# Performance work log

Measured on AMD Instinct MI355X. Metric: run time of the kernel, lower is better.

Reference implementation:

```python
import jax, jax.numpy as jnp
import numpy as np
from jax import lax

GRID_SIZE = 5
SPLINE_ORDER = 3
N_COEF = GRID_SIZE + SPLINE_ORDER  # 8 b-spline basis functions per input
GRID_LO, GRID_HI = -1.0, 1.0


def _grid():
    h = (GRID_HI - GRID_LO) / GRID_SIZE
    return jnp.arange(-SPLINE_ORDER, GRID_SIZE + SPLINE_ORDER + 1, dtype=jnp.float32) * h + GRID_LO


def _bsplines(x):
    # x: [..., in] -> [..., in, N_COEF] via Cox-de Boor recursion (efficient-kan)
    grid = _grid()
    x = x[..., None]
    bases = ((x >= grid[:-1]) & (x < grid[1:])).astype(x.dtype)
    for j in range(1, SPLINE_ORDER + 1):
        bases = ((x - grid[:-(j + 1)]) / (grid[j:-1] - grid[:-(j + 1)]) * bases[..., :-1]
                 + (grid[j + 1:] - x) / (grid[j + 1:] - grid[1:-j]) * bases[..., 1:])
    return bases


def _kan_linear(x, base_w, spline_w):
    # x: [..., in]; base_w: [out, in]; spline_w: [out, in, N_COEF]
    base = jax.nn.silu(x) @ base_w.T
    b = _bsplines(x).reshape(x.shape[:-1] + (-1,))  # [..., in*N_COEF]
    return base + b @ spline_w.reshape(spline_w.shape[0], -1).T


def _kan_conv(x, base_w, spline_w):
    # x: [B, C, H, W]; 3x3 valid KAN convolution
    patches = lax.conv_general_dilated_patches(x, (3, 3), (1, 1), 'VALID')  # [B, C*9, H-2, W-2]
    p = patches.transpose(0, 2, 3, 1)  # [B, Ho, Wo, C*9]
    out = _kan_linear(p, base_w, spline_w)  # [B, Ho, Wo, out]
    return out.transpose(0, 3, 1, 2)


def _maxpool2(x):
    return lax.reduce_window(x, -jnp.inf, lax.max, (1, 1, 2, 2), (1, 1, 2, 2), 'VALID')


def setup_inputs() -> dict:
    key = jax.random.key(0)
    ks = jax.random.split(key, 12)
    B = 2048
    x = jax.random.uniform(ks[0], (B, 1, 28, 28), dtype=jnp.float32)
    s = 0.1
    return {
        'x': x,
        'bw1': jax.random.normal(ks[1], (5, 9), dtype=jnp.float32) * s,
        'sw1': jax.random.normal(ks[2], (5, 9, N_COEF), dtype=jnp.float32) * s,
        'bw2': jax.random.normal(ks[3], (5, 45), dtype=jnp.float32) * s,
        'sw2': jax.random.normal(ks[4], (5, 45, N_COEF), dtype=jnp.float32) * s,
        'bw3': jax.random.normal(ks[5], (2, 45), dtype=jnp.float32) * s,
        'sw3': jax.random.normal(ks[6], (2, 45, N_COEF), dtype=jnp.float32) * s,
        'w1': jax.random.normal(ks[7], (500, 162), dtype=jnp.float32) * 0.05,
        'b1': jnp.zeros((500,), dtype=jnp.float32),
        'w2': jax.random.normal(ks[8], (10, 500), dtype=jnp.float32) * 0.05,
        'b2': jnp.zeros((10,), dtype=jnp.float32),
    }


def reference(x, bw1, sw1, bw2, sw2, bw3, sw3, w1, b1, w2, b2):
    h = _kan_conv(x, bw1, sw1)       # [B, 5, 26, 26]
    h = _maxpool2(h)                 # [B, 5, 13, 13]
    h = _kan_conv(h, bw2, sw2)       # [B, 5, 11, 11]
    h = _kan_conv(h, bw3, sw3)       # [B, 2, 9, 9]
    h = h.reshape(h.shape[0], -1)    # [B, 162]
    h = jax.nn.relu(h @ w1.T + b1)   # [B, 500]
    return h @ w2.T + b2             # [B, 10]
```

## Files before the change

### kernel.cpp

```cpp
#include <hip/hip_runtime.h>


typedef _Float16 h2 __attribute__((ext_vector_type(2)));

__device__ __forceinline__ h2 u2h(unsigned int u) {
  union { unsigned int x; h2 h; } v; v.x = u; return v.h;
}
__device__ __forceinline__ unsigned short f2h_bits(float x) {
  union { _Float16 h; unsigned short u; } v; v.h = (_Float16)x; return v.u;
}
__device__ __forceinline__ unsigned int pack2h(float a, float b) {
  return (unsigned int)f2h_bits(a) | ((unsigned int)f2h_bits(b) << 16);
}
__device__ __forceinline__ float fdot2(h2 a, h2 b, float c) {
  return __builtin_amdgcn_fdot2(a, b, c, false);
}

__device__ __forceinline__ void featurize_regs(float v, uint4& bs, float& silu) {
  silu = v / (1.0f + __expf(-v));
  bs.x = 0u; bs.y = 0u; bs.z = 0u; bs.w = 0u;
  float u = fmaf(v, 2.5f, 5.5f);
  if (u >= 0.0f && u < 11.0f) {
    float tf = floorf(u);
    float f = u - tf, f2 = f * f, f3 = f2 * f, om = 1.0f - f;
    const float c6 = 1.0f / 6.0f;
    float w0 = om * om * om * c6;
    float w1 = (3.0f * f3 - 6.0f * f2 + 4.0f) * c6;
    float w2 = (-3.0f * f3 + 3.0f * f2 + 3.0f * f + 1.0f) * c6;
    float w3 = f3 * c6;
    unsigned long long w01 =
        (unsigned long long)f2h_bits(w0) |
        ((unsigned long long)f2h_bits(w1) << 16) |
        ((unsigned long long)f2h_bits(w2) << 32) |
        ((unsigned long long)f2h_bits(w3) << 48);
    int t = (int)tf;
    int s = 16 * t - 48;
    unsigned long long lo, hi;
    if (s >= 0) {
      lo = (s < 64) ? (w01 << s) : 0ull;
      hi = (s == 0) ? 0ull : ((s < 64) ? (w01 >> (64 - s)) : (w01 << (s - 64)));
    } else {
      lo = w01 >> (-s);
      hi = 0ull;
    }
    bs.x = (unsigned int)lo; bs.y = (unsigned int)(lo >> 32);
    bs.z = (unsigned int)hi; bs.w = (unsigned int)(hi >> 32);
  }
}

__global__ __launch_bounds__(256) void k_prep(
    const float* __restrict__ bw1, const float* __restrict__ sw1,
    const float* __restrict__ bw2, const float* __restrict__ sw2,
    const float* __restrict__ bw3, const float* __restrict__ sw3,
    const float* __restrict__ w1, const float* __restrict__ w2,
    unsigned int* __restrict__ V1s, float* __restrict__ V1b,
    unsigned int* __restrict__ V2s, float* __restrict__ V2b,
    unsigned int* __restrict__ V3s, float* __restrict__ V3b,
    unsigned int* __restrict__ W1p4, float* __restrict__ W2p) {
  int t = blockIdx.x * 256 + threadIdx.x;
  if (t < 180) {
    int p = t & 3, o = (t >> 2) % 5, in = t / 20;
    V1s[t] = pack2h(sw1[(o * 9 + in) * 8 + 2 * p], sw1[(o * 9 + in) * 8 + 2 * p + 1]);
  }
  if (t < 45)  { int o = t % 5, in = t / 5; V1b[t] = bw1[o * 9 + in]; }
  if (t < 900) {
    int p = t & 3, o = (t >> 2) % 5, in = t / 20;
    V2s[t] = pack2h(sw2[(o * 45 + in) * 8 + 2 * p], sw2[(o * 45 + in) * 8 + 2 * p + 1]);
  }
  if (t < 225) { int o = t % 5, in = t / 5; V2b[t] = bw2[o * 45 + in]; }
  if (t < 360) {
    int p = t & 3, o = (t >> 2) & 1, in = t / 8;
    V3s[t] = pack2h(sw3[(o * 45 + in) * 8 + 2 * p], sw3[(o * 45 + in) * 8 + 2 * p + 1]);
  }
  if (t < 90)  { int o = t % 2, in = t / 2; V3b[t] = bw3[o * 45 + in]; }
  if (t < 43008) {
    int j = t & 3, o = (t >> 2) & 511, kpq = t >> 11;
    int kp = kpq * 4 + j;
    W1p4[t] = (o < 500 && kp < 81)
                  ? pack2h(w1[o * 162 + 2 * kp], w1[o * 162 + 2 * kp + 1])
                  : 0u;
  }
  if (t < 5120) {
    int o = t >> 9, k = t & 511;
    W2p[t] = (k < 500) ? w2[o * 500 + k] : 0.0f;
  }
}

__global__ __launch_bounds__(64, 2) void k_fused(
    const float* __restrict__ x,
    const unsigned int* __restrict__ V1s, const float* __restrict__ V1b,
    const unsigned int* __restrict__ V2s, const float* __restrict__ V2b,
    const unsigned int* __restrict__ V3s, const float* __restrict__ V3b,
    const unsigned int* __restrict__ W1p4, const float* __restrict__ W2p,
    const float* __restrict__ b1, const float* __restrict__ b2,
    float* __restrict__ out) {
  __shared__ uint4 bas[845];
  __shared__ float slu[845];
  float*        basF = (float*)bas;
  unsigned int* hpk  = (unsigned int*)slu + 256;
  const int b = blockIdx.x;
  const int lane = threadIdx.x;

  for (int l = lane; l < 784; l += 64) {
    uint4 bs; float sl;
    featurize_regs(x[b * 784 + l], bs, sl);
    bas[l] = bs; slu[l] = sl;
  }

  float h1v[3][5];
  #pragma unroll 1
  for (int it = 0; it < 3; ++it) {
    int p = it * 64 + lane;
    if (p < 169) {
      int py = p / 13, px = p % 13;
      int r0 = py * 2, c0 = px * 2;
      float wacc[4][5];
      #pragma unroll
      for (int wi = 0; wi < 4; ++wi)
        #pragma unroll
        for (int o = 0; o < 5; ++o) wacc[wi][o] = 0.0f;
      #pragma unroll
      for (int r = 0; r < 4; ++r) {
        uint4 q[4]; float sl[4];
        #pragma unroll
        for (int c = 0; c < 4; ++c) {
          q[c]  = bas[(r0 + r) * 28 + c0 + c];
          sl[c] = slu[(r0 + r) * 28 + c0 + c];
        }
        #pragma unroll
        for (int c = 0; c < 4; ++c) {
          h2 a0 = u2h(q[c].x), a1 = u2h(q[c].y), a2 = u2h(q[c].z), a3 = u2h(q[c].w);
          #pragma unroll
          for (int dy = 0; dy < 2; ++dy) {
            #pragma unroll
            for (int dx = 0; dx < 2; ++dx) {
              int ky = r - dy, kx = c - dx;
              if (ky >= 0 && ky < 3 && kx >= 0 && kx < 3) {
                const unsigned int* wp = V1s + (ky * 3 + kx) * 20;
                const float* bp = V1b + (ky * 3 + kx) * 5;
                #pragma unroll
                for (int o = 0; o < 5; ++o) {
                  float acc = wacc[dy * 2 + dx][o];
                  acc = fdot2(a0, u2h(wp[o * 4 + 0]), acc);
                  acc = fdot2(a1, u2h(wp[o * 4 + 1]), acc);
                  acc = fdot2(a2, u2h(wp[o * 4 + 2]), acc);
                  acc = fdot2(a3, u2h(wp[o * 4 + 3]), acc);
                  wacc[dy * 2 + dx][o] = fmaf(sl[c], bp[o], acc);
                }
              }
            }
          }
        }
      }
      #pragma unroll
      for (int o = 0; o < 5; ++o)
        h1v[it][o] = fmaxf(fmaxf(wacc[0][o], wacc[1][o]),
                           fmaxf(wacc[2][o], wacc[3][o]));
    }
  }
  #pragma unroll 1
  for (int it = 0; it < 3; ++it) {
    int p = it * 64 + lane;
    if (p < 169) {
      #pragma unroll
      for (int o = 0; o < 5; ++o) {
        uint4 bs; float sl;
        featurize_regs(h1v[it][o], bs, sl);
        bas[o * 169 + p] = bs; slu[o * 169 + p] = sl;
      }
    }
  }

  float h2v[2][5];
  #pragma unroll 1
  for (int it = 0; it < 2; ++it) {
    int pos = it * 64 + lane;
    if (pos < 121) {
      int y = pos / 11, xx = pos % 11;
      float acc2[5];
      #pragma unroll
      for (int o = 0; o < 5; ++o) acc2[o] = 0.0f;
      #pragma unroll 1
      for (int cky = 0; cky < 15; ++cky) {
        int c = cky / 3, ky = cky % 3;
        int base = c * 169 + (y + ky) * 13 + xx;
        uint4 q0 = bas[base], q1 = bas[base + 1], q2 = bas[base + 2];
        float s0 = slu[base], s1 = slu[base + 1], s2 = slu[base + 2];
        uint4 wq[15]; float wb[15];
        const uint4* wp4 = (const uint4*)(V2s + cky * 60);
        const float* bp  = V2b + cky * 15;
        #pragma unroll
        for (int i = 0; i < 15; ++i) { wq[i] = wp4[i]; wb[i] = bp[i]; }
        #pragma unroll
        for (int kx = 0; kx < 3; ++kx) {
          uint4 q = (kx == 0) ? q0 : ((kx == 1) ? q1 : q2);
          float sl = (kx == 0) ? s0 : ((kx == 1) ? s1 : s2);
          h2 a0 = u2h(q.x), a1 = u2h(q.y), a2 = u2h(q.z), a3 = u2h(q.w);
          #pragma unroll
          for (int o = 0; o < 5; ++o) {
            uint4 w = wq[kx * 5 + o];
            float a = acc2[o];
            a = fdot2(a0, u2h(w.x), a);
            a = fdot2(a1, u2h(w.y), a);
            a = fdot2(a2, u2h(w.z), a);
            a = fdot2(a3, u2h(w.w), a);
            acc2[o] = fmaf(sl, wb[kx * 5 + o], a);
          }
        }
      }
      #pragma unroll
      for (int o = 0; o < 5; ++o) h2v[it][o] = acc2[o];
    }
  }
  #pragma unroll 1
  for (int it = 0; it < 2; ++it) {
    int pos = it * 64 + lane;
    if (pos < 121) {
      #pragma unroll
      for (int o = 0; o < 5; ++o) {
        uint4 bs; float sl;
        featurize_regs(h2v[it][o], bs, sl);
        bas[o * 121 + pos] = bs; slu[o * 121 + pos] = sl;
      }
    }
  }

  float h3v[2][2];
  #pragma unroll 1
  for (int it = 0; it < 2; ++it) {
    int pos = it * 64 + lane;
    if (pos < 81) {
      int y = pos / 9, xx = pos % 9;
      float acc3[2] = {0.f, 0.f};
      #pragma unroll 1
      for (int cky = 0; cky < 15; ++cky) {
        int c = cky / 3, ky = cky % 3;
        int base = c * 121 + (y + ky) * 11 + xx;
        uint4 q0 = bas[base], q1 = bas[base + 1], q2 = bas[base + 2];
        float s0 = slu[base], s1 = slu[base + 1], s2 = slu[base + 2];
        uint4 wq[6]; float wb[6];
        const uint4* wp4 = (const uint4*)(V3s + cky * 24);
        const float* bp  = V3b + cky * 6;
        #pragma unroll
        for (int i = 0; i < 6; ++i) { wq[i] = wp4[i]; wb[i] = bp[i]; }
        #pragma unroll
        for (int kx = 0; kx < 3; ++kx) {
          uint4 q = (kx == 0) ? q0 : ((kx == 1) ? q1 : q2);
          float sl = (kx == 0) ? s0 : ((kx == 1) ? s1 : s2);
          h2 a0 = u2h(q.x), a1 = u2h(q.y), a2 = u2h(q.z), a3 = u2h(q.w);
          #pragma unroll
          for (int o = 0; o < 2; ++o) {
            uint4 w = wq[kx * 2 + o];
            float a = acc3[o];
            a = fdot2(a0, u2h(w.x), a);
            a = fdot2(a1, u2h(w.y), a);
            a = fdot2(a2, u2h(w.z), a);
            a = fdot2(a3, u2h(w.w), a);
            acc3[o] = fmaf(sl, wb[kx * 2 + o], a);
          }
        }
      }
      h3v[it][0] = acc3[0]; h3v[it][1] = acc3[1];
    }
  }
  #pragma unroll 1
  for (int it = 0; it < 2; ++it) {
    int pos = it * 64 + lane;
    if (pos < 81) { slu[pos] = h3v[it][0]; slu[81 + pos] = h3v[it][1]; }
  }
  hpk[lane] = pack2h(slu[2 * lane], slu[2 * lane + 1]);
  {
    int i1 = 64 + lane;
    if (i1 < 84)
      hpk[i1] = (i1 < 81) ? pack2h(slu[2 * i1], slu[2 * i1 + 1]) : 0u;
  }

  float fa[8];
  #pragma unroll
  for (int i = 0; i < 8; ++i) fa[i] = 0.0f;
  {
    const uint4* hp4 = (const uint4*)hpk;
    #pragma unroll 1
    for (int kpq = 0; kpq < 21; ++kpq) {
      uint4 hk = hp4[kpq];
      const uint4* wrow = (const uint4*)W1p4 + kpq * 512 + lane;
      #pragma unroll
      for (int i = 0; i < 8; ++i) {
        uint4 wv = wrow[i * 64];
        float a = fa[i];
        a = fdot2(u2h(hk.x), u2h(wv.x), a);
        a = fdot2(u2h(hk.y), u2h(wv.y), a);
        a = fdot2(u2h(hk.z), u2h(wv.z), a);
        a = fdot2(u2h(hk.w), u2h(wv.w), a);
        fa[i] = a;
      }
    }
  }
  #pragma unroll
  for (int i = 0; i < 8; ++i) {
    int o = lane + 64 * i;
    float bb = (o < 500) ? b1[o] : 0.0f;
    float v = fa[i] + bb;
    basF[o] = (v > 0.0f && o < 500) ? v : 0.0f;
  }

  float hv0, hv1, hv2, hv3, hv4, hv5, hv6, hv7;
  {
    const float4* hf = (const float4*)&basF[lane * 8];
    float4 ha = hf[0], hb = hf[1];
    hv0 = ha.x; hv1 = ha.y; hv2 = ha.z; hv3 = ha.w;
    hv4 = hb.x; hv5 = hb.y; hv6 = hb.z; hv7 = hb.w;
  }
  float acc10[10];
  #pragma unroll
  for (int o = 0; o < 10; ++o) {
    const float4* wp = (const float4*)&W2p[o * 512 + lane * 8];
    float4 w0 = wp[0], w1v = wp[1];
    float s = hv0 * w0.x + hv1 * w0.y + hv2 * w0.z + hv3 * w0.w;
    s += hv4 * w1v.x + hv5 * w1v.y + hv6 * w1v.z + hv7 * w1v.w;
    acc10[o] = s;
  }
  #pragma unroll
  for (int off = 32; off > 0; off >>= 1) {
    #pragma unroll
    for (int o = 0; o < 10; ++o) acc10[o] += __shfl_down(acc10[o], off);
  }
  if (lane == 0) {
    #pragma unroll
    for (int o = 0; o < 10; ++o) out[b * 10 + o] = acc10[o] + b2[o];
  }
}

extern "C" void kernel_launch(void* const* d_in, const int* in_sizes, int n_in,
                              void* d_out, int out_size, void* d_ws, size_t ws_size,
                              hipStream_t stream) {
  (void)in_sizes; (void)n_in; (void)out_size; (void)ws_size;
  const float* x   = (const float*)d_in[0];
  const float* bw1 = (const float*)d_in[1];
  const float* sw1 = (const float*)d_in[2];
  const float* bw2 = (const float*)d_in[3];
  const float* sw2 = (const float*)d_in[4];
  const float* bw3 = (const float*)d_in[5];
  const float* sw3 = (const float*)d_in[6];
  const float* w1  = (const float*)d_in[7];
  const float* b1  = (const float*)d_in[8];
  const float* w2  = (const float*)d_in[9];
  const float* b2  = (const float*)d_in[10];
  float* out = (float*)d_out;

  char* ws = (char*)d_ws;
  unsigned int* V1s  = (unsigned int*)(ws);
  float*        V1b  = (float*)(ws + 768);
  unsigned int* V2s  = (unsigned int*)(ws + 1024);
  float*        V2b  = (float*)(ws + 4672);
  unsigned int* V3s  = (unsigned int*)(ws + 5632);
  float*        V3b  = (float*)(ws + 7168);
  float*        W2p  = (float*)(ws + 7680);
  unsigned int* W1p4 = (unsigned int*)(ws + 28672);

  k_prep<<<168, 256, 0, stream>>>(bw1, sw1, bw2, sw2, bw3, sw3, w1, w2,
                                  V1s, V1b, V2s, V2b, V3s, V3b, W1p4, W2p);
  k_fused<<<2048, 64, 0, stream>>>(x, V1s, V1b, V2s, V2b, V3s, V3b,
                                   W1p4, W2p, b1, b2, out);
}
```

Baseline: 136.8 us.

## Double-buffer FC1 weight loads, merge conv2/conv3 position loops, store SiLU as fp16

Result: no change. 136.5 us (-0.2%).

```diff
diff --git a/kernel.cpp b/kernel.cpp
--- a/kernel.cpp
+++ b/kernel.cpp
@@ -8,6 +8,9 @@
 }
 __device__ __forceinline__ unsigned short f2h_bits(float x) {
   union { _Float16 h; unsigned short u; } v; v.h = (_Float16)x; return v.u;
+}
+__device__ __forceinline__ float h2f(unsigned short u) {
+  union { unsigned short u; _Float16 h; } v; v.u = u; return (float)v.h;
 }
 __device__ __forceinline__ unsigned int pack2h(float a, float b) {
   return (unsigned int)f2h_bits(a) | ((unsigned int)f2h_bits(b) << 16);
@@ -74,8 +77,8 @@
   }
   if (t < 90)  { int o = t % 2, in = t / 2; V3b[t] = bw3[o * 45 + in]; }
   if (t < 43008) {
-    int j = t & 3, o = (t >> 2) & 511, kpq = t >> 11;
-    int kp = kpq * 4 + j;
+    int j = t & 3, o = (t >> 2) & 511, g = t >> 11;
+    int kp = g * 4 + j;
     W1p4[t] = (o < 500 && kp < 81)
                   ? pack2h(w1[o * 162 + 2 * kp], w1[o * 162 + 2 * kp + 1])
                   : 0u;
@@ -95,16 +98,18 @@
     const float* __restrict__ b1, const float* __restrict__ b2,
     float* __restrict__ out) {
   __shared__ uint4 bas[845];
-  __shared__ float slu[845];
+  __shared__ unsigned short slu16[848];
   float*        basF = (float*)bas;
-  unsigned int* hpk  = (unsigned int*)slu + 256;
+  float*        h3f  = basF + 2048;
+  unsigned int* hpk  = (unsigned int*)basF + 2560;
   const int b = blockIdx.x;
   const int lane = threadIdx.x;
 
+  #pragma unroll 1
   for (int l = lane; l < 784; l += 64) {
     uint4 bs; float sl;
     featurize_regs(x[b * 784 + l], bs, sl);
-    bas[l] = bs; slu[l] = sl;
+    bas[l] = bs; slu16[l] = f2h_bits(sl);
   }
 
   float h1v[3][5];
@@ -125,7 +130,7 @@
         #pragma unroll
         for (int c = 0; c < 4; ++c) {
           q[c]  = bas[(r0 + r) * 28 + c0 + c];
-          sl[c] = slu[(r0 + r) * 28 + c0 + c];
+          sl[c] = h2f(slu16[(r0 + r) * 28 + c0 + c]);
         }
         #pragma unroll
         for (int c = 0; c < 4; ++c) {
@@ -166,113 +171,127 @@
       for (int o = 0; o < 5; ++o) {
         uint4 bs; float sl;
         featurize_regs(h1v[it][o], bs, sl);
-        bas[o * 169 + p] = bs; slu[o * 169 + p] = sl;
-      }
-    }
-  }
-
-  float h2v[2][5];
-  #pragma unroll 1
-  for (int it = 0; it < 2; ++it) {
-    int pos = it * 64 + lane;
-    if (pos < 121) {
-      int y = pos / 11, xx = pos % 11;
-      float acc2[5];
-      #pragma unroll
-      for (int o = 0; o < 5; ++o) acc2[o] = 0.0f;
-      #pragma unroll 1
-      for (int cky = 0; cky < 15; ++cky) {
-        int c = cky / 3, ky = cky % 3;
-        int base = c * 169 + (y + ky) * 13 + xx;
-        uint4 q0 = bas[base], q1 = bas[base + 1], q2 = bas[base + 2];
-        float s0 = slu[base], s1 = slu[base + 1], s2 = slu[base + 2];
-        uint4 wq[15]; float wb[15];
-        const uint4* wp4 = (const uint4*)(V2s + cky * 60);
-        const float* bp  = V2b + cky * 15;
-        #pragma unroll
-        for (int i = 0; i < 15; ++i) { wq[i] = wp4[i]; wb[i] = bp[i]; }
+        bas[o * 169 + p] = bs; slu16[o * 169 + p] = f2h_bits(sl);
+      }
+    }
+  }
+
+  float acc2[2][5];
+  {
+    #pragma unroll
+    for (int ct = 0; ct < 2; ++ct)
+      #pragma unroll
+      for (int o = 0; o < 5; ++o) acc2[ct][o] = 0.0f;
+    int pos0 = lane;
+    int y0 = pos0 / 11, x0 = pos0 % 11;
+    int pos1 = 64 + lane;
+    int p1c = (pos1 < 121) ? pos1 : 120;
+    int y1 = p1c / 11, x1 = p1c % 11;
+    #pragma unroll 1
+    for (int cky = 0; cky < 15; ++cky) {
+      int c = cky / 3, ky = cky - c * 3;
+      int ba0 = c * 169 + (y0 + ky) * 13 + x0;
+      int ba1 = c * 169 + (y1 + ky) * 13 + x1;
+      uint4 q00 = bas[ba0], q01 = bas[ba0 + 1], q02 = bas[ba0 + 2];
+      uint4 q10 = bas[ba1], q11 = bas[ba1 + 1], q12 = bas[ba1 + 2];
+      float s00 = h2f(slu16[ba0]), s01 = h2f(slu16[ba0 + 1]), s02 = h2f(slu16[ba0 + 2]);
+      float s10 = h2f(slu16[ba1]), s11 = h2f(slu16[ba1 + 1]), s12 = h2f(slu16[ba1 + 2]);
+      uint4 wq[15]; float wb[15];
+      const uint4* wp4 = (const uint4*)(V2s + cky * 60);
+      const float* bp  = V2b + cky * 15;
+      #pragma unroll
+      for (int i = 0; i < 15; ++i) { wq[i] = wp4[i]; wb[i] = bp[i]; }
+      #pragma unroll
+      for (int ct = 0; ct < 2; ++ct) {
         #pragma unroll
         for (int kx = 0; kx < 3; ++kx) {
-          uint4 q = (kx == 0) ? q0 : ((kx == 1) ? q1 : q2);
-          float sl = (kx == 0) ? s0 : ((kx == 1) ? s1 : s2);
+          uint4 q = ct ? ((kx == 0) ? q10 : ((kx == 1) ? q11 : q12))
+                       : ((kx == 0) ? q00 : ((kx == 1) ? q01 : q02));
+          float sl = ct ? ((kx == 0) ? s10 : ((kx == 1) ? s11 : s12))
+                        : ((kx == 0) ? s00 : ((kx == 1) ? s01 : s02));
           h2 a0 = u2h(q.x), a1 = u2h(q.y), a2 = u2h(q.z), a3 = u2h(q.w);
           #pragma unroll
           for (int o = 0; o < 5; ++o) {
             uint4 w = wq[kx * 5 + o];
-            float a = acc2[o];
+            float a = acc2[ct][o];
             a = fdot2(a0, u2h(w.x), a);
             a = fdot2(a1, u2h(w.y), a);
             a = fdot2(a2, u2h(w.z), a);
             a = fdot2(a3, u2h(w.w), a);
-            acc2[o] = fmaf(sl, wb[kx * 5 + o], a);
+            acc2[ct][o] = fmaf(sl, wb[kx * 5 + o], a);
           }
         }
       }
-      #pragma unroll
-      for (int o = 0; o < 5; ++o) h2v[it][o] = acc2[o];
     }
   }
   #pragma unroll 1
-  for (int it = 0; it < 2; ++it) {
-    int pos = it * 64 + lane;
+  for (int ct = 0; ct < 2; ++ct) {
+    int pos = ct * 64 + lane;
     if (pos < 121) {
       #pragma unroll
       for (int o = 0; o < 5; ++o) {
         uint4 bs; float sl;
-        featurize_regs(h2v[it][o], bs, sl);
-        bas[o * 121 + pos] = bs; slu[o * 121 + pos] = sl;
-      }
-    }
-  }
-
-  float h3v[2][2];
-  #pragma unroll 1
-  for (int it = 0; it < 2; ++it) {
-    int pos = it * 64 + lane;
-    if (pos < 81) {
-      int y = pos / 9, xx = pos % 9;
-      float acc3[2] = {0.f, 0.f};
-      #pragma unroll 1
-      for (int cky = 0; cky < 15; ++cky) {
-        int c = cky / 3, ky = cky % 3;
-        int base = c * 121 + (y + ky) * 11 + xx;
-        uint4 q0 = bas[base], q1 = bas[base + 1], q2 = bas[base + 2];
-        float s0 = slu[base], s1 = slu[base + 1], s2 = slu[base + 2];
-        uint4 wq[6]; float wb[6];
-        const uint4* wp4 = (const uint4*)(V3s + cky * 24);
-        const float* bp  = V3b + cky * 6;
-        #pragma unroll
-        for (int i = 0; i < 6; ++i) { wq[i] = wp4[i]; wb[i] = bp[i]; }
+        featurize_regs(acc2[ct][o], bs, sl);
+        bas[o * 121 + pos] = bs; slu16[o * 121 + pos] = f2h_bits(sl);
+      }
+    }
+  }
+
+  float acc3[2][2];
+  {
+    acc3[0][0] = acc3[0][1] = acc3[1][0] = acc3[1][1] = 0.0f;
+    int pos0 = lane;
+    int y0 = pos0 / 9, x0 = pos0 % 9;
+    int pos1 = 64 + lane;
+    int p1c = (pos1 < 81) ? pos1 : 80;
+    int y1 = p1c / 9, x1 = p1c % 9;
+    #pragma unroll 1
+    for (int cky = 0; cky < 15; ++cky) {
+      int c = cky / 3, ky = cky - c * 3;
+      int ba0 = c * 121 + (y0 + ky) * 11 + x0;
+      int ba1 = c * 121 + (y1 + ky) * 11 + x1;
+      uint4 q00 = bas[ba0], q01 = bas[ba0 + 1], q02 = bas[ba0 + 2];
+      uint4 q10 = bas[ba1], q11 = bas[ba1 + 1], q12 = bas[ba1 + 2];
+      float s00 = h2f(slu16[ba0]), s01 = h2f(slu16[ba0 + 1]), s02 = h2f(slu16[ba0 + 2]);
+      float s10 = h2f(slu16[ba1]), s11 = h2f(slu16[ba1 + 1]), s12 = h2f(slu16[ba1 + 2]);
+      uint4 wq[6]; float wb[6];
+      const uint4* wp4 = (const uint4*)(V3s + cky * 24);
+      const float* bp  = V3b + cky * 6;
+      #pragma unroll
+      for (int i = 0; i < 6; ++i) { wq[i] = wp4[i]; wb[i] = bp[i]; }
+      #pragma unroll
+      for (int ct = 0; ct < 2; ++ct) {
         #pragma unroll
         for (int kx = 0; kx < 3; ++kx) {
-          uint4 q = (kx == 0) ? q0 : ((kx == 1) ? q1 : q2);
-          float sl = (kx == 0) ? s0 : ((kx == 1) ? s1 : s2);
+          uint4 q = ct ? ((kx == 0) ? q10 : ((kx == 1) ? q11 : q12))
+                       : ((kx == 0) ? q00 : ((kx == 1) ? q01 : q02));
+          float sl = ct ? ((kx == 0) ? s10 : ((kx == 1) ? s11 : s12))
+                        : ((kx == 0) ? s00 : ((kx == 1) ? s01 : s02));
           h2 a0 = u2h(q.x), a1 = u2h(q.y), a2 = u2h(q.z), a3 = u2h(q.w);
           #pragma unroll
           for (int o = 0; o < 2; ++o) {
             uint4 w = wq[kx * 2 + o];
-            float a = acc3[o];
+            float a = acc3[ct][o];
             a = fdot2(a0, u2h(w.x), a);
             a = fdot2(a1, u2h(w.y), a);
             a = fdot2(a2, u2h(w.z), a);
             a = fdot2(a3, u2h(w.w), a);
-            acc3[o] = fmaf(sl, wb[kx * 2 + o], a);
+            acc3[ct][o] = fmaf(sl, wb[kx * 2 + o], a);
           }
         }
       }
-      h3v[it][0] = acc3[0]; h3v[it][1] = acc3[1];
     }
   }
   #pragma unroll 1
-  for (int it = 0; it < 2; ++it) {
-    int pos = it * 64 + lane;
-    if (pos < 81) { slu[pos] = h3v[it][0]; slu[81 + pos] = h3v[it][1]; }
-  }
-  hpk[lane] = pack2h(slu[2 * lane], slu[2 * lane + 1]);
+  for (int ct = 0; ct < 2; ++ct) {
+    int pos = ct * 64 + lane;
+    if (pos < 81) { h3f[pos] = acc3[ct][0]; h3f[81 + pos] = acc3[ct][1]; }
+  }
+  hpk[lane] = pack2h(h3f[2 * lane], h3f[2 * lane + 1]);
   {
     int i1 = 64 + lane;
     if (i1 < 84)
-      hpk[i1] = (i1 < 81) ? pack2h(slu[2 * i1], slu[2 * i1 + 1]) : 0u;
+      hpk[i1] = (i1 < 81) ? pack2h(h3f[2 * i1], h3f[2 * i1 + 1]) : 0u;
   }
 
   float fa[8];
@@ -280,19 +299,45 @@
   for (int i = 0; i < 8; ++i) fa[i] = 0.0f;
   {
     const uint4* hp4 = (const uint4*)hpk;
+    const uint4* wbase = (const uint4*)W1p4 + lane;
+    uint4 wA[8], wB[8];
+    #pragma unroll
+    for (int i = 0; i < 8; ++i) wA[i] = wbase[i * 64];
     #pragma unroll 1
-    for (int kpq = 0; kpq < 21; ++kpq) {
-      uint4 hk = hp4[kpq];
-      const uint4* wrow = (const uint4*)W1p4 + kpq * 512 + lane;
-      #pragma unroll
-      for (int i = 0; i < 8; ++i) {
-        uint4 wv = wrow[i * 64];
-        float a = fa[i];
-        a = fdot2(u2h(hk.x), u2h(wv.x), a);
-        a = fdot2(u2h(hk.y), u2h(wv.y), a);
-        a = fdot2(u2h(hk.z), u2h(wv.z), a);
-        a = fdot2(u2h(hk.w), u2h(wv.w), a);
-        fa[i] = a;
+    for (int g = 0; g < 21; g += 2) {
+      if (g + 1 < 21) {
+        const uint4* p = wbase + (g + 1) * 512;
+        #pragma unroll
+        for (int i = 0; i < 8; ++i) wB[i] = p[i * 64];
+      }
+      {
+        uint4 hk = hp4[g];
+        #pragma unroll
+        for (int i = 0; i < 8; ++i) {
+          float a = fa[i];
+          a = fdot2(u2h(hk.x), u2h(wA[i].x), a);
+          a = fdot2(u2h(hk.y), u2h(wA[i].y), a);
+          a = fdot2(u2h(hk.z), u2h(wA[i].z), a);
+          a = fdot2(u2h(hk.w), u2h(wA[i].w), a);
+          fa[i] = a;
+        }
+      }
+      if (g + 2 < 21) {
+        const uint4* p = wbase + (g + 2) * 512;
+        #pragma unroll
+        for (int i = 0; i < 8; ++i) wA[i] = p[i * 64];
+      }
+      if (g + 1 < 21) {
+        uint4 hk = hp4[g + 1];
+        #pragma unroll
+        for (int i = 0; i < 8; ++i) {
+          float a = fa[i];
+          a = fdot2(u2h(hk.x), u2h(wB[i].x), a);
+          a = fdot2(u2h(hk.y), u2h(wB[i].y), a);
+          a = fdot2(u2h(hk.z), u2h(wB[i].z), a);
+          a = fdot2(u2h(hk.w), u2h(wB[i].w), a);
+          fa[i] = a;
+        }
       }
     }
   }
```
